# Kernel optimization log

Measured on AMD Instinct MI355X. Metric: run time of the kernel, lower is better.

The kernel has to match this reference:

```python
import jax, jax.numpy as jnp
import numpy as np

NUM_HEADS = 12

def _elu1(x):
    return jax.nn.elu(x) + 1.0

def setup_inputs() -> dict:
    key = jax.random.key(0)
    ks = jax.random.split(key, 7)
    B, Nq, Nk, D = 8, 4096, 1024, 768
    s = 0.02
    return {
        "x_query": jax.random.normal(ks[0], (B, Nq, D), dtype=jnp.float32),
        "x_key_value": jax.random.normal(ks[1], (B, Nk, D), dtype=jnp.float32),
        "Wq": jax.random.normal(ks[2], (D, D), dtype=jnp.float32) * s,
        "Wk": jax.random.normal(ks[3], (D, D), dtype=jnp.float32) * s,
        "Wv": jax.random.normal(ks[4], (D, D), dtype=jnp.float32) * s,
        "Wo": jax.random.normal(ks[5], (D, D), dtype=jnp.float32) * s,
        "bo": jax.random.normal(ks[6], (D,), dtype=jnp.float32) * s,
    }

def reference(x_query, x_key_value, Wq, Wk, Wv, Wo, bo):
    B, Nq, D = x_query.shape
    Nk = x_key_value.shape[1]
    H = NUM_HEADS
    hd = D // H
    # projections (torch Linear: x @ W.T), split heads -> [B, H, N, hd]
    q = (x_query @ Wq.T).reshape(B, Nq, H, hd).transpose(0, 2, 1, 3)
    k = (x_key_value @ Wk.T).reshape(B, Nk, H, hd).transpose(0, 2, 1, 3)
    v = (x_key_value @ Wv.T).reshape(B, Nk, H, hd).transpose(0, 2, 1, 3)
    q = _elu1(q)
    k = _elu1(k)
    # kv: [B,H,hd,hd]; k_sum: [B,H,hd]
    kv = jnp.einsum('bhnd,bhne->bhde', k, v)
    k_sum = k.sum(axis=2)
    z = 1.0 / (jnp.einsum('bhqd,bhd->bhq', q, k_sum) + 1e-6)  # [B,H,Nq]
    attn_out = jnp.einsum('bhqd,bhde->bhqe', q, kv) * z[..., None]
    attn_out = attn_out.transpose(0, 2, 1, 3).reshape(B, Nq, D)
    return attn_out @ Wo.T + bo
```

## Files before the change

### kernel.cpp

```cpp
#include <hip/hip_runtime.h>

typedef _Float16 half8_t __attribute__((ext_vector_type(8)));
typedef _Float16 half4_t __attribute__((ext_vector_type(4)));
typedef float    float4_t __attribute__((ext_vector_type(4)));

#define DIM 768

#define GLOAD16(g, l) __builtin_amdgcn_global_load_lds(                        \
    (const __attribute__((address_space(1))) void*)(g),                        \
    (__attribute__((address_space(3))) void*)(l), 16, 0, 0)

#define MFMA16(a, b, c) __builtin_amdgcn_mfma_f32_16x16x32_f16((a), (b), (c), 0, 0, 0)

__global__ __launch_bounds__(256) void cast_f32_f16(const float* __restrict__ s,
                                                    _Float16* __restrict__ d, int n8)
{
    int i = blockIdx.x * 256 + threadIdx.x;
    if (i < n8) {
        float4_t f0 = *(const float4_t*)&s[(size_t)i * 8];
        float4_t f1 = *(const float4_t*)&s[(size_t)i * 8 + 4];
        half8_t h;
        #pragma unroll
        for (int e = 0; e < 4; ++e) { h[e] = (_Float16)f0[e]; h[e + 4] = (_Float16)f1[e]; }
        *(half8_t*)&d[(size_t)i * 8] = h;
    }
}

__global__ __launch_bounds__(256) void cast4_f32_f16(
    const float* __restrict__ s0, const float* __restrict__ s1,
    const float* __restrict__ s2, const float* __restrict__ s3,
    _Float16* __restrict__ d0, _Float16* __restrict__ d1,
    _Float16* __restrict__ d2, _Float16* __restrict__ d3)
{
    const float* s; _Float16* d;
    switch (blockIdx.y) {
        case 0: s = s0; d = d0; break;
        case 1: s = s1; d = d1; break;
        case 2: s = s2; d = d2; break;
        default: s = s3; d = d3; break;
    }
    int i = blockIdx.x * 256 + threadIdx.x;
    float4_t f0 = *(const float4_t*)&s[(size_t)i * 8];
    float4_t f1 = *(const float4_t*)&s[(size_t)i * 8 + 4];
    half8_t h;
    #pragma unroll
    for (int e = 0; e < 4; ++e) { h[e] = (_Float16)f0[e]; h[e + 4] = (_Float16)f1[e]; }
    *(half8_t*)&d[(size_t)i * 8] = h;
}

__device__ __forceinline__ void gemm_core(const _Float16* __restrict__ A,
                                          const _Float16* __restrict__ W,
                                          int row0, int col0, _Float16* lds,
                                          float4_t acc[4][4])
{
    const int tid  = threadIdx.x;
    const int wid  = tid >> 6, lane = tid & 63;
    const int wr   = wid >> 1;
    const int wc   = wid & 1;

    const int srow  = lane & 15;
    const int skoct = lane >> 4;
    const _Float16* As0 = A + (size_t)(row0 + wid * 32 + srow)      * DIM + skoct * 8;
    const _Float16* As1 = A + (size_t)(row0 + wid * 32 + 16 + srow) * DIM + skoct * 8;
    const _Float16* Bs0 = W + (size_t)(col0 + wid * 16 + srow)      * DIM + skoct * 8;

#define STAGE(t, s) do {                                                      \
        GLOAD16(As0 + (t) * 32, &lds[(s) * 12288 + (2 * wid) * 512]);         \
        GLOAD16(As1 + (t) * 32, &lds[(s) * 12288 + (2 * wid + 1) * 512]);     \
        GLOAD16(Bs0 + (t) * 32, &lds[(s) * 12288 + 8192 + wid * 512]);        \
    } while (0)

    const int aoff = (wr * 4) * 512 + lane * 8;
    const int boff = 8192 + (wc * 4) * 512 + lane * 8;

    STAGE(0, 0);
    STAGE(1, 1);
    asm volatile("s_waitcnt vmcnt(3)" ::: "memory");
    __builtin_amdgcn_s_barrier();
    __builtin_amdgcn_sched_barrier(0);

    int s = 0, s2 = 2;
    for (int t = 0; t < 24; ++t) {
        const _Float16* sl = &lds[s * 12288];
        half8_t af[4], bf[4];
        #pragma unroll
        for (int mi = 0; mi < 4; ++mi)
            af[mi] = *(const half8_t*)&sl[aoff + mi * 512];
        #pragma unroll
        for (int ni = 0; ni < 4; ++ni)
            bf[ni] = *(const half8_t*)&sl[boff + ni * 512];
        if (t < 22) STAGE(t + 2, s2);

        __builtin_amdgcn_s_setprio(1);
        #pragma unroll
        for (int mi = 0; mi < 4; ++mi)
            #pragma unroll
            for (int ni = 0; ni < 4; ++ni)
                acc[mi][ni] = MFMA16(af[mi], bf[ni], acc[mi][ni]);
        __builtin_amdgcn_s_setprio(0);

        if (t < 23) {
            __builtin_amdgcn_sched_barrier(0);
            if (t < 22) asm volatile("s_waitcnt vmcnt(3)" ::: "memory");
            else        asm volatile("s_waitcnt vmcnt(0)" ::: "memory");
            __builtin_amdgcn_s_barrier();
            __builtin_amdgcn_sched_barrier(0);
        }
        s  = (s  == 2) ? 0 : s  + 1;
        s2 = (s2 == 2) ? 0 : s2 + 1;
    }
#undef STAGE
}

__global__ __launch_bounds__(512, 4) void proj_qkv(
    const _Float16* __restrict__ xq16, const _Float16* __restrict__ xkv16,
    const _Float16* __restrict__ Wq16, const _Float16* __restrict__ Wk16,
    const _Float16* __restrict__ Wv16,
    _Float16* __restrict__ q16, _Float16* __restrict__ k16,
    _Float16* __restrict__ v16)
{
    __shared__ __align__(16) _Float16 lds[3 * 12288];

    const int cpx = gridDim.x >> 3;
    int bid = (blockIdx.x & 7) * cpx + (blockIdx.x >> 3);

    const _Float16 *A, *W;
    _Float16 *O;
    bool elu;
    int brow, bcol;
    if (bid < 768) {
        A = xq16; W = Wq16; O = q16; elu = true;
        brow = bid / 6; bcol = bid - brow * 6;
    } else {
        int u = bid - 768;
        int mat = u / 192;  u -= mat * 192;
        A = xkv16; W = mat ? Wv16 : Wk16; O = mat ? v16 : k16; elu = !mat;
        brow = u / 6; bcol = u - brow * 6;
    }
    const int row0 = brow * 256, col0 = bcol * 128;

    float4_t acc[4][4] = {};
    gemm_core(A, W, row0, col0, lds, acc);

    const int wid = threadIdx.x >> 6, lane = threadIdx.x & 63;
    const int wr = wid >> 1, wc = wid & 1, lr = lane & 15, lkg = lane >> 4;
    #pragma unroll
    for (int mi = 0; mi < 4; ++mi) {
        #pragma unroll
        for (int ni = 0; ni < 4; ++ni) {
            #pragma unroll
            for (int e = 0; e < 4; ++e) {
                int r = row0 + wr * 64 + mi * 16 + lkg * 4 + e;
                int c = col0 + wc * 64 + ni * 16 + lr;
                float v = acc[mi][ni][e];
                if (elu) v = (v > 0.0f) ? (v + 1.0f) : __expf(v);
                O[(size_t)r * DIM + c] = (_Float16)v;
            }
        }
    }
}

__global__ __launch_bounds__(512, 4) void out_proj(
    const _Float16* __restrict__ a16, const _Float16* __restrict__ Wo16,
    const float* __restrict__ bo, float* __restrict__ out)
{
    __shared__ __align__(16) _Float16 lds[3 * 12288];

    const int cpx = gridDim.x >> 3;
    int bid = (blockIdx.x & 7) * cpx + (blockIdx.x >> 3);
    const int brow = bid / 6, bcol = bid - brow * 6;
    const int row0 = brow * 256, col0 = bcol * 128;

    float4_t acc[4][4] = {};
    gemm_core(a16, Wo16, row0, col0, lds, acc);

    const int wid = threadIdx.x >> 6, lane = threadIdx.x & 63;
    const int wr = wid >> 1, wc = wid & 1, lr = lane & 15, lkg = lane >> 4;
    #pragma unroll
    for (int mi = 0; mi < 4; ++mi) {
        #pragma unroll
        for (int ni = 0; ni < 4; ++ni) {
            #pragma unroll
            for (int e = 0; e < 4; ++e) {
                int r = row0 + wr * 64 + mi * 16 + lkg * 4 + e;
                int c = col0 + wc * 64 + ni * 16 + lr;
                out[(size_t)r * DIM + c] = acc[mi][ni][e] + bo[c];
            }
        }
    }
}

__global__ __launch_bounds__(256) void kv_reduce(const _Float16* __restrict__ k16,
                                                 const _Float16* __restrict__ v16,
                                                 float* __restrict__ kvh,
                                                 float* __restrict__ ksum)
{
    __shared__ __align__(16) _Float16 K[128][64];
    __shared__ __align__(16) _Float16 V[128][64];
    const int chunk = blockIdx.x;
    const int bh    = blockIdx.y;
    const int b = bh / 12, h = bh % 12;
    const int tid = threadIdx.x;

    const size_t base = ((size_t)b * 1024 + (size_t)chunk * 128) * DIM + h * 64;
    #pragma unroll
    for (int j = 0; j < 4; ++j) {
        int idx = j * 256 + tid;
        int r = idx >> 3, c = (idx & 7) * 8;
        *(half8_t*)&K[r][c] = *(const half8_t*)&k16[base + (size_t)r * DIM + c];
        *(half8_t*)&V[r][c] = *(const half8_t*)&v16[base + (size_t)r * DIM + c];
    }
    __syncthreads();

    const int d0 = (tid & 15) * 4;
    const int e0 = (tid >> 4) * 4;
    float acc[4][4] = {};
    #pragma unroll 4
    for (int n = 0; n < 128; ++n) {
        half4_t kd = *(const half4_t*)&K[n][d0];
        half4_t ve = *(const half4_t*)&V[n][e0];
        #pragma unroll
        for (int i = 0; i < 4; ++i)
            #pragma unroll
            for (int j = 0; j < 4; ++j)
                acc[i][j] += (float)ve[i] * (float)kd[j];
    }
    float* kvp = kvh + (size_t)bh * 64 * 64;
    #pragma unroll
    for (int i = 0; i < 4; ++i)
        #pragma unroll
        for (int j = 0; j < 4; ++j)
            atomicAdd(&kvp[(e0 + i) * 64 + d0 + j], acc[i][j]);

    if (tid < 64) {
        float s = 0.0f;
        for (int n = 0; n < 128; ++n) s += (float)K[n][tid];
        atomicAdd(&ksum[bh * 64 + tid], s);
    }
}

__global__ __launch_bounds__(256) void attn_kernel(_Float16* __restrict__ q16,
                                                   const float* __restrict__ kvh,
                                                   const float* __restrict__ ksum)
{
    __shared__ __align__(16) _Float16 Q[128][72];
    __shared__ __align__(16) _Float16 Bv[64][72];
    __shared__ float S[64];
    __shared__ float Z[128];

    const int h    = blockIdx.x;
    const int rb   = blockIdx.y;
    const int row0 = rb * 128;
    const int b    = row0 >> 12;
    const int bh   = b * 12 + h;
    const int tid  = threadIdx.x;

    #pragma unroll
    for (int j = 0; j < 4; ++j) {
        int idx = j * 256 + tid;
        int r = idx >> 3, c = (idx & 7) * 8;
        *(half8_t*)&Q[r][c] =
            *(const half8_t*)&q16[(size_t)(row0 + r) * DIM + h * 64 + c];
    }
    #pragma unroll
    for (int j = 0; j < 4; ++j) {
        int idx = j * 256 + tid;
        int r = idx >> 4, c = (idx & 15) * 4;
        float4_t f = *(const float4_t*)&kvh[((size_t)bh * 64 + r) * 64 + c];
        half4_t hh;
        #pragma unroll
        for (int e = 0; e < 4; ++e) hh[e] = (_Float16)f[e];
        *(half4_t*)&Bv[r][c] = hh;
    }
    if (tid < 64) S[tid] = ksum[bh * 64 + tid];
    __syncthreads();

    if (tid < 128) {
        float dot = 0.0f;
        #pragma unroll 8
        for (int d = 0; d < 64; ++d) dot += (float)Q[tid][d] * S[d];
        Z[tid] = 1.0f / (dot + 1e-6f);
    }
    __syncthreads();

    const int w = tid >> 6, lane = tid & 63;
    const int lr = lane & 15, lkg = lane >> 4;
    float4_t acc[2][4] = {};
    #pragma unroll
    for (int kc = 0; kc < 2; ++kc) {
        half8_t aF[2], bF[4];
        #pragma unroll
        for (int mi = 0; mi < 2; ++mi)
            aF[mi] = *(const half8_t*)&Q[w * 32 + mi * 16 + lr][kc * 32 + lkg * 8];
        #pragma unroll
        for (int ni = 0; ni < 4; ++ni)
            bF[ni] = *(const half8_t*)&Bv[ni * 16 + lr][kc * 32 + lkg * 8];
        #pragma unroll
        for (int mi = 0; mi < 2; ++mi)
            #pragma unroll
            for (int ni = 0; ni < 4; ++ni)
                acc[mi][ni] = MFMA16(aF[mi], bF[ni], acc[mi][ni]);
    }
    #pragma unroll
    for (int mi = 0; mi < 2; ++mi) {
        #pragma unroll
        for (int ni = 0; ni < 4; ++ni) {
            #pragma unroll
            for (int e = 0; e < 4; ++e) {
                int r = w * 32 + mi * 16 + lkg * 4 + e;
                float v = acc[mi][ni][e] * Z[r];
                q16[(size_t)(row0 + r) * DIM + h * 64 + ni * 16 + lr] = (_Float16)v;
            }
        }
    }
}

extern "C" void kernel_launch(void* const* d_in, const int* in_sizes, int n_in,
                              void* d_out, int out_size, void* d_ws, size_t ws_size,
                              hipStream_t stream)
{
    const float* xq  = (const float*)d_in[0];
    const float* xkv = (const float*)d_in[1];
    const float* Wq  = (const float*)d_in[2];
    const float* Wk  = (const float*)d_in[3];
    const float* Wv  = (const float*)d_in[4];
    const float* Wo  = (const float*)d_in[5];
    const float* bo  = (const float*)d_in[6];

    char* ws = (char*)d_ws;
    const size_t SZ_XKV16 = (size_t)8192 * 768 * 2;
    const size_t SZ_Q16   = (size_t)32768 * 768 * 2;
    const size_t SZ_W16   = (size_t)768 * 768 * 2;
    const size_t SZ_KVH   = (size_t)96 * 64 * 64 * 4;
    const size_t SZ_KSUM  = (size_t)96 * 64 * 4;

    _Float16* xkv16 = (_Float16*)(ws);
    _Float16* q16   = (_Float16*)(ws + SZ_XKV16);
    _Float16* Wq16  = (_Float16*)(ws + SZ_XKV16 + SZ_Q16);
    _Float16* Wk16  = (_Float16*)(ws + SZ_XKV16 + SZ_Q16 + SZ_W16);
    _Float16* Wv16  = (_Float16*)(ws + SZ_XKV16 + SZ_Q16 + 2 * SZ_W16);
    _Float16* Wo16  = (_Float16*)(ws + SZ_XKV16 + SZ_Q16 + 3 * SZ_W16);
    float*    kvh   = (float*)   (ws + SZ_XKV16 + SZ_Q16 + 4 * SZ_W16);
    float*    ksum  = (float*)   (ws + SZ_XKV16 + SZ_Q16 + 4 * SZ_W16 + SZ_KVH);

    char* ob = (char*)d_out;
    _Float16* xq16 = (_Float16*)(ob);
    _Float16* k16  = (_Float16*)(ob + 50331648);
    _Float16* v16  = (_Float16*)(ob + 50331648 + 12582912);
    float*    out  = (float*)d_out;

    cast_f32_f16<<<12288, 256, 0, stream>>>(xq,  xq16,  3145728);
    cast_f32_f16<<< 3072, 256, 0, stream>>>(xkv, xkv16,  786432);
    cast4_f32_f16<<<dim3(288, 4), 256, 0, stream>>>(Wq, Wk, Wv, Wo,
                                                    Wq16, Wk16, Wv16, Wo16);
    hipMemsetAsync(kvh, 0, SZ_KVH + SZ_KSUM, stream);

    proj_qkv<<<1152, 512, 0, stream>>>(xq16, xkv16, Wq16, Wk16, Wv16,
                                       q16, k16, v16);

    kv_reduce<<<dim3(8, 96), 256, 0, stream>>>(k16, v16, kvh, ksum);
    attn_kernel<<<dim3(12, 256), 256, 0, stream>>>(q16, kvh, ksum);

    out_proj<<<768, 512, 0, stream>>>(q16, Wo16, bo, out);
}
```

Measured before the change: 259.9 us.

## Fuse fp32-to-fp16 activation cast into projection GEMM and retile to 64-wide K steps

Drops the separate cast kernels for x_query and x_key_value. The QKV projection GEMM now loads fp32 activations straight into registers, converts them to fp16 and writes them to LDS itself, which removes a full round trip of the large activation tensors through global memory. The GEMM core is also restructured: K steps are 64 wide, warps are laid out 2x4 with 8x2 accumulators, double LDS buffers are larger, and the occupancy hint is removed. The cost is higher register and LDS pressure, extra barriers per tile, and manual conversion work sitting inside the main loop.

```diff
diff --git a/kernel.cpp b/kernel.cpp
--- a/kernel.cpp
+++ b/kernel.cpp
@@ -11,20 +11,6 @@
     (__attribute__((address_space(3))) void*)(l), 16, 0, 0)
 
 #define MFMA16(a, b, c) __builtin_amdgcn_mfma_f32_16x16x32_f16((a), (b), (c), 0, 0, 0)
-
-__global__ __launch_bounds__(256) void cast_f32_f16(const float* __restrict__ s,
-                                                    _Float16* __restrict__ d, int n8)
-{
-    int i = blockIdx.x * 256 + threadIdx.x;
-    if (i < n8) {
-        float4_t f0 = *(const float4_t*)&s[(size_t)i * 8];
-        float4_t f1 = *(const float4_t*)&s[(size_t)i * 8 + 4];
-        half8_t h;
-        #pragma unroll
-        for (int e = 0; e < 4; ++e) { h[e] = (_Float16)f0[e]; h[e + 4] = (_Float16)f1[e]; }
-        *(half8_t*)&d[(size_t)i * 8] = h;
-    }
-}
 
 __global__ __launch_bounds__(256) void cast4_f32_f16(
     const float* __restrict__ s0, const float* __restrict__ s1,
@@ -48,110 +34,253 @@
     *(half8_t*)&d[(size_t)i * 8] = h;
 }
 
-__device__ __forceinline__ void gemm_core(const _Float16* __restrict__ A,
+template<bool AF32>
+__device__ __forceinline__ void gemm_core(const void* __restrict__ Av,
                                           const _Float16* __restrict__ W,
-                                          int row0, int col0, _Float16* lds,
-                                          float4_t acc[4][4])
+                                          int row0, int col0,
+                                          _Float16* lds, float4_t acc[8][2])
 {
     const int tid  = threadIdx.x;
     const int wid  = tid >> 6, lane = tid & 63;
-    const int wr   = wid >> 1;
-    const int wc   = wid & 1;
-
-    const int srow  = lane & 15;
-    const int skoct = lane >> 4;
-    const _Float16* As0 = A + (size_t)(row0 + wid * 32 + srow)      * DIM + skoct * 8;
-    const _Float16* As1 = A + (size_t)(row0 + wid * 32 + 16 + srow) * DIM + skoct * 8;
-    const _Float16* Bs0 = W + (size_t)(col0 + wid * 16 + srow)      * DIM + skoct * 8;
-
-#define STAGE(t, s) do {                                                      \
-        GLOAD16(As0 + (t) * 32, &lds[(s) * 12288 + (2 * wid) * 512]);         \
-        GLOAD16(As1 + (t) * 32, &lds[(s) * 12288 + (2 * wid + 1) * 512]);     \
-        GLOAD16(Bs0 + (t) * 32, &lds[(s) * 12288 + 8192 + wid * 512]);        \
-    } while (0)
-
-    const int aoff = (wr * 4) * 512 + lane * 8;
-    const int boff = 8192 + (wc * 4) * 512 + lane * 8;
-
-    STAGE(0, 0);
-    STAGE(1, 1);
-    asm volatile("s_waitcnt vmcnt(3)" ::: "memory");
-    __builtin_amdgcn_s_barrier();
-    __builtin_amdgcn_sched_barrier(0);
-
-    int s = 0, s2 = 2;
-    for (int t = 0; t < 24; ++t) {
-        const _Float16* sl = &lds[s * 12288];
-        half8_t af[4], bf[4];
-        #pragma unroll
-        for (int mi = 0; mi < 4; ++mi)
-            af[mi] = *(const half8_t*)&sl[aoff + mi * 512];
-        #pragma unroll
-        for (int ni = 0; ni < 4; ++ni)
-            bf[ni] = *(const half8_t*)&sl[boff + ni * 512];
-        if (t < 22) STAGE(t + 2, s2);
-
-        __builtin_amdgcn_s_setprio(1);
-        #pragma unroll
-        for (int mi = 0; mi < 4; ++mi)
-            #pragma unroll
-            for (int ni = 0; ni < 4; ++ni)
-                acc[mi][ni] = MFMA16(af[mi], bf[ni], acc[mi][ni]);
-        __builtin_amdgcn_s_setprio(0);
-
-        if (t < 23) {
+    const int wr   = wid >> 2, wc = wid & 3;
+
+    const _Float16* Bst = W + (size_t)(col0 + wid * 16 + (lane & 15)) * DIM
+                            + (lane >> 4) * 8;
+
+    const int aoffs = (wr * 8) * 1024 + lane * 8;
+    const int boffs = 16384 + (wc * 2) * 1024 + lane * 8;
+
+    const _Float16* Ah = nullptr;
+    const float*    Af = nullptr;
+    int awr = 0;
+    if constexpr (AF32) {
+        const int rg = 2 * wid + (lane >> 5);
+        const int j  = lane & 31;
+        const int row = j & 15, q = j >> 4;
+        Af  = (const float*)Av + (size_t)(row0 + rg * 16 + row) * DIM + q * 32;
+        awr = (rg * 2 + q) * 512 + row * 8;
+    } else {
+        Ah = (const _Float16*)Av + (size_t)(row0 + 2 * wid * 16 + (lane & 15)) * DIM
+                                 + (lane >> 4) * 8;
+    }
+
+#define B_STAGE(t, s) do {                                                     \
+        GLOAD16(Bst + (t) * 64,      &lds[(s) * 24576 + 16384 + (2*wid  ) * 512]); \
+        GLOAD16(Bst + (t) * 64 + 32, &lds[(s) * 24576 + 16384 + (2*wid+1) * 512]); \
+    } while (0)
+
+#define AH_STAGE(t, s) do {                                                    \
+        GLOAD16(Ah + (t)*64,              &lds[(s)*24576 + (4*wid  )*512]);    \
+        GLOAD16(Ah + (t)*64 + 32,         &lds[(s)*24576 + (4*wid+1)*512]);    \
+        GLOAD16(Ah + (t)*64 + 16*DIM,     &lds[(s)*24576 + (4*wid+2)*512]);    \
+        GLOAD16(Ah + (t)*64 + 16*DIM+32,  &lds[(s)*24576 + (4*wid+3)*512]);    \
+    } while (0)
+
+#define AF_ISSUE(t, R) do { _Pragma("unroll")                                  \
+        for (int i = 0; i < 8; ++i)                                            \
+            R[i] = *(const float4_t*)(Af + (t) * 64 + i * 4);                  \
+    } while (0)
+
+#define AF_WRITE(s1w, R) do {                                                  \
+        _Float16* dst = &lds[(s1w) * 24576 + awr];                             \
+        _Pragma("unroll") for (int p = 0; p < 4; ++p) {                        \
+            half8_t h;                                                         \
+            _Pragma("unroll") for (int e = 0; e < 4; ++e) {                    \
+                h[e] = (_Float16)R[2*p][e]; h[4+e] = (_Float16)R[2*p+1][e]; }  \
+            *(half8_t*)&dst[p * 128] = h; }                                    \
+    } while (0)
+
+#define READ_BF(s) do {                                                        \
+        bf[0][0] = *(const half8_t*)&lds[(s)*24576 + boffs];                   \
+        bf[0][1] = *(const half8_t*)&lds[(s)*24576 + boffs + 512];             \
+        bf[1][0] = *(const half8_t*)&lds[(s)*24576 + boffs + 1024];            \
+        bf[1][1] = *(const half8_t*)&lds[(s)*24576 + boffs + 1536];            \
+    } while (0)
+
+#define READ_AFR(af, s, mb) do { _Pragma("unroll")                             \
+        for (int i = 0; i < 4; ++i) {                                          \
+            af[i][0] = *(const half8_t*)&lds[(s)*24576 + aoffs + ((mb)+i)*1024];       \
+            af[i][1] = *(const half8_t*)&lds[(s)*24576 + aoffs + ((mb)+i)*1024 + 512]; \
+        } } while (0)
+
+#define MMA4(base, af) do {                                                    \
+        asm volatile("s_waitcnt lgkmcnt(0)" ::: "memory");                     \
+        __builtin_amdgcn_sched_barrier(0);                                     \
+        __builtin_amdgcn_s_setprio(1);                                         \
+        _Pragma("unroll") for (int i = 0; i < 4; ++i)                          \
+            _Pragma("unroll") for (int n2 = 0; n2 < 2; ++n2) {                 \
+                acc[(base)+i][n2] = MFMA16(af[i][0], bf[n2][0], acc[(base)+i][n2]); \
+                acc[(base)+i][n2] = MFMA16(af[i][1], bf[n2][1], acc[(base)+i][n2]); \
+            }                                                                  \
+        __builtin_amdgcn_s_setprio(0);                                         \
+        __builtin_amdgcn_sched_barrier(0);                                     \
+    } while (0)
+
+    if constexpr (AF32) {
+        float4_t Ra[8], Rb[8];
+        AF_ISSUE(0, Ra); B_STAGE(0, 0);
+        __builtin_amdgcn_sched_barrier(0);
+        AF_ISSUE(1, Rb); B_STAGE(1, 1);
+        __builtin_amdgcn_sched_barrier(0);
+        asm volatile("s_waitcnt vmcnt(10)" ::: "memory");
+        AF_WRITE(0, Ra);
+        asm volatile("s_waitcnt lgkmcnt(0)" ::: "memory");
+        __builtin_amdgcn_sched_barrier(0);
+        __builtin_amdgcn_s_barrier();
+
+#define TILE_F32(t, Ri, Rw) do {                                               \
+        const int s = (t) % 3, s1 = ((t)+1) % 3, s2 = ((t)+2) % 3;             \
+        __builtin_amdgcn_sched_barrier(0);                                     \
+        half8_t bf[2][2];                                                      \
+        READ_BF(s);                                                            \
+        { half8_t af[4][2]; READ_AFR(af, s, 0);                                \
+          AF_ISSUE((t)+2, Ri); B_STAGE((t)+2, s2);                             \
+          __builtin_amdgcn_s_barrier();                                        \
+          MMA4(0, af);                                                         \
+          __builtin_amdgcn_s_barrier(); }                                      \
+        { half8_t af[4][2]; READ_AFR(af, s, 4);                                \
+          asm volatile("s_waitcnt vmcnt(10)" ::: "memory");                    \
+          AF_WRITE(s1, Rw);                                                    \
+          __builtin_amdgcn_s_barrier();                                        \
+          MMA4(4, af);                                                         \
+          __builtin_amdgcn_s_barrier(); }                                      \
+    } while (0)
+
+        #pragma unroll
+        for (int t = 0; t < 10; t += 2) {
+            TILE_F32(t,     Ra, Rb);
+            TILE_F32(t + 1, Rb, Ra);
+        }
+        {
             __builtin_amdgcn_sched_barrier(0);
-            if (t < 22) asm volatile("s_waitcnt vmcnt(3)" ::: "memory");
-            else        asm volatile("s_waitcnt vmcnt(0)" ::: "memory");
-            __builtin_amdgcn_s_barrier();
+            half8_t bf[2][2];
+            READ_BF(1);
+            { half8_t af[4][2]; READ_AFR(af, 1, 0);
+              __builtin_amdgcn_s_barrier();
+              MMA4(0, af);
+              __builtin_amdgcn_s_barrier(); }
+            { half8_t af[4][2]; READ_AFR(af, 1, 4);
+              asm volatile("s_waitcnt vmcnt(0)" ::: "memory");
+              AF_WRITE(2, Rb);
+              __builtin_amdgcn_s_barrier();
+              MMA4(4, af);
+              __builtin_amdgcn_s_barrier(); }
+        }
+        {
             __builtin_amdgcn_sched_barrier(0);
-        }
-        s  = (s  == 2) ? 0 : s  + 1;
-        s2 = (s2 == 2) ? 0 : s2 + 1;
-    }
-#undef STAGE
-}
-
-__global__ __launch_bounds__(512, 4) void proj_qkv(
-    const _Float16* __restrict__ xq16, const _Float16* __restrict__ xkv16,
+            half8_t bf[2][2];
+            READ_BF(2);
+            { half8_t af[4][2]; READ_AFR(af, 2, 0);
+              __builtin_amdgcn_s_barrier();
+              MMA4(0, af);
+              __builtin_amdgcn_s_barrier(); }
+            { half8_t af[4][2]; READ_AFR(af, 2, 4);
+              __builtin_amdgcn_s_barrier();
+              MMA4(4, af); }
+        }
+#undef TILE_F32
+    } else {
+        AH_STAGE(0, 0); B_STAGE(0, 0);
+        __builtin_amdgcn_sched_barrier(0);
+        AH_STAGE(1, 1); B_STAGE(1, 1);
+        __builtin_amdgcn_sched_barrier(0);
+        asm volatile("s_waitcnt vmcnt(6)" ::: "memory");
+        __builtin_amdgcn_s_barrier();
+
+#define TILE_H16(t) do {                                                       \
+        const int s = (t) % 3, s2 = ((t)+2) % 3;                               \
+        __builtin_amdgcn_sched_barrier(0);                                     \
+        half8_t bf[2][2];                                                      \
+        READ_BF(s);                                                            \
+        { half8_t af[4][2]; READ_AFR(af, s, 0);                                \
+          AH_STAGE((t)+2, s2); B_STAGE((t)+2, s2);                             \
+          __builtin_amdgcn_s_barrier();                                        \
+          MMA4(0, af);                                                         \
+          __builtin_amdgcn_s_barrier(); }                                      \
+        { half8_t af[4][2]; READ_AFR(af, s, 4);                                \
+          __builtin_amdgcn_s_barrier();                                        \
+          MMA4(4, af);                                                         \
+          asm volatile("s_waitcnt vmcnt(6)" ::: "memory");                     \
+          __builtin_amdgcn_s_barrier(); }                                      \
+    } while (0)
+
+        #pragma unroll
+        for (int t = 0; t < 10; ++t) TILE_H16(t);
+        {
+            __builtin_amdgcn_sched_barrier(0);
+            half8_t bf[2][2];
+            READ_BF(1);
+            { half8_t af[4][2]; READ_AFR(af, 1, 0);
+              __builtin_amdgcn_s_barrier();
+              MMA4(0, af);
+              __builtin_amdgcn_s_barrier(); }
+            { half8_t af[4][2]; READ_AFR(af, 1, 4);
+              __builtin_amdgcn_s_barrier();
+              MMA4(4, af);
+              asm volatile("s_waitcnt vmcnt(0)" ::: "memory");
+              __builtin_amdgcn_s_barrier(); }
+        }
+        {
+            __builtin_amdgcn_sched_barrier(0);
+            half8_t bf[2][2];
+            READ_BF(2);
+            { half8_t af[4][2]; READ_AFR(af, 2, 0);
+              __builtin_amdgcn_s_barrier();
+              MMA4(0, af);
+              __builtin_amdgcn_s_barrier(); }
+            { half8_t af[4][2]; READ_AFR(af, 2, 4);
+              __builtin_amdgcn_s_barrier();
+              MMA4(4, af); }
+        }
+#undef TILE_H16
+    }
+#undef B_STAGE
+#undef AH_STAGE
+#undef AF_ISSUE
+#undef AF_WRITE
+#undef READ_BF
+#undef READ_AFR
+#undef MMA4
+}
+
+__global__ __launch_bounds__(512) void proj_qkv(
+    const float* __restrict__ xq, const float* __restrict__ xkv,
     const _Float16* __restrict__ Wq16, const _Float16* __restrict__ Wk16,
     const _Float16* __restrict__ Wv16,
     _Float16* __restrict__ q16, _Float16* __restrict__ k16,
     _Float16* __restrict__ v16)
 {
-    __shared__ __align__(16) _Float16 lds[3 * 12288];
+    __shared__ __align__(16) _Float16 lds[3 * 24576];
 
     const int cpx = gridDim.x >> 3;
     int bid = (blockIdx.x & 7) * cpx + (blockIdx.x >> 3);
 
-    const _Float16 *A, *W;
-    _Float16 *O;
-    bool elu;
+    const float* A; const _Float16* W; _Float16* O; bool elu;
     int brow, bcol;
     if (bid < 768) {
-        A = xq16; W = Wq16; O = q16; elu = true;
+        A = xq; W = Wq16; O = q16; elu = true;
         brow = bid / 6; bcol = bid - brow * 6;
     } else {
         int u = bid - 768;
         int mat = u / 192;  u -= mat * 192;
-        A = xkv16; W = mat ? Wv16 : Wk16; O = mat ? v16 : k16; elu = !mat;
+        A = xkv; W = mat ? Wv16 : Wk16; O = mat ? v16 : k16; elu = !mat;
         brow = u / 6; bcol = u - brow * 6;
     }
     const int row0 = brow * 256, col0 = bcol * 128;
 
-    float4_t acc[4][4] = {};
-    gemm_core(A, W, row0, col0, lds, acc);
+    float4_t acc[8][2] = {};
+    gemm_core<true>(A, W, row0, col0, lds, acc);
 
     const int wid = threadIdx.x >> 6, lane = threadIdx.x & 63;
-    const int wr = wid >> 1, wc = wid & 1, lr = lane & 15, lkg = lane >> 4;
-    #pragma unroll
-    for (int mi = 0; mi < 4; ++mi) {
-        #pragma unroll
-        for (int ni = 0; ni < 4; ++ni) {
+    const int wr = wid >> 2, wc = wid & 3, lr = lane & 15, lkg = lane >> 4;
+    #pragma unroll
+    for (int mi = 0; mi < 8; ++mi) {
+        #pragma unroll
+        for (int ni = 0; ni < 2; ++ni) {
             #pragma unroll
             for (int e = 0; e < 4; ++e) {
-                int r = row0 + wr * 64 + mi * 16 + lkg * 4 + e;
-                int c = col0 + wc * 64 + ni * 16 + lr;
+                int r = row0 + wr * 128 + mi * 16 + lkg * 4 + e;
+                int c = col0 + wc * 32 + ni * 16 + lr;
                 float v = acc[mi][ni][e];
                 if (elu) v = (v > 0.0f) ? (v + 1.0f) : __expf(v);
                 O[(size_t)r * DIM + c] = (_Float16)v;
@@ -160,30 +289,30 @@
     }
 }
 
-__global__ __launch_bounds__(512, 4) void out_proj(
+__global__ __launch_bounds__(512) void out_proj(
     const _Float16* __restrict__ a16, const _Float16* __restrict__ Wo16,
     const float* __restrict__ bo, float* __restrict__ out)
 {
-    __shared__ __align__(16) _Float16 lds[3 * 12288];
+    __shared__ __align__(16) _Float16 lds[3 * 24576];
 
     const int cpx = gridDim.x >> 3;
     int bid = (blockIdx.x & 7) * cpx + (blockIdx.x >> 3);
     const int brow = bid / 6, bcol = bid - brow * 6;
     const int row0 = brow * 256, col0 = bcol * 128;
 
-    float4_t acc[4][4] = {};
-    gemm_core(a16, Wo16, row0, col0, lds, acc);
+    float4_t acc[8][2] = {};
+    gemm_core<false>(a16, Wo16, row0, col0, lds, acc);
 
     const int wid = threadIdx.x >> 6, lane = threadIdx.x & 63;
-    const int wr = wid >> 1, wc = wid & 1, lr = lane & 15, lkg = lane >> 4;
-    #pragma unroll
-    for (int mi = 0; mi < 4; ++mi) {
-        #pragma unroll
-        for (int ni = 0; ni < 4; ++ni) {
+    const int wr = wid >> 2, wc = wid & 3, lr = lane & 15, lkg = lane >> 4;
+    #pragma unroll
+    for (int mi = 0; mi < 8; ++mi) {
+        #pragma unroll
+        for (int ni = 0; ni < 2; ++ni) {
             #pragma unroll
             for (int e = 0; e < 4; ++e) {
-                int r = row0 + wr * 64 + mi * 16 + lkg * 4 + e;
-                int c = col0 + wc * 64 + ni * 16 + lr;
+                int r = row0 + wr * 128 + mi * 16 + lkg * 4 + e;
+                int c = col0 + wc * 32 + ni * 16 + lr;
                 out[(size_t)r * DIM + c] = acc[mi][ni][e] + bo[c];
             }
         }
@@ -328,34 +457,29 @@
     const float* bo  = (const float*)d_in[6];
 
     char* ws = (char*)d_ws;
-    const size_t SZ_XKV16 = (size_t)8192 * 768 * 2;
-    const size_t SZ_Q16   = (size_t)32768 * 768 * 2;
-    const size_t SZ_W16   = (size_t)768 * 768 * 2;
-    const size_t SZ_KVH   = (size_t)96 * 64 * 64 * 4;
-    const size_t SZ_KSUM  = (size_t)96 * 64 * 4;
-
-    _Float16* xkv16 = (_Float16*)(ws);
-    _Float16* q16   = (_Float16*)(ws + SZ_XKV16);
-    _Float16* Wq16  = (_Float16*)(ws + SZ_XKV16 + SZ_Q16);
-    _Float16* Wk16  = (_Float16*)(ws + SZ_XKV16 + SZ_Q16 + SZ_W16);
-    _Float16* Wv16  = (_Float16*)(ws + SZ_XKV16 + SZ_Q16 + 2 * SZ_W16);
-    _Float16* Wo16  = (_Float16*)(ws + SZ_XKV16 + SZ_Q16 + 3 * SZ_W16);
-    float*    kvh   = (float*)   (ws + SZ_XKV16 + SZ_Q16 + 4 * SZ_W16);
-    float*    ksum  = (float*)   (ws + SZ_XKV16 + SZ_Q16 + 4 * SZ_W16 + SZ_KVH);
+    const size_t SZ_Q16  = (size_t)32768 * 768 * 2;
+    const size_t SZ_W16  = (size_t)768 * 768 * 2;
+    const size_t SZ_KVH  = (size_t)96 * 64 * 64 * 4;
+    const size_t SZ_KSUM = (size_t)96 * 64 * 4;
+
+    _Float16* q16  = (_Float16*)(ws);
+    _Float16* Wq16 = (_Float16*)(ws + SZ_Q16);
+    _Float16* Wk16 = (_Float16*)(ws + SZ_Q16 + SZ_W16);
+    _Float16* Wv16 = (_Float16*)(ws + SZ_Q16 + 2 * SZ_W16);
+    _Float16* Wo16 = (_Float16*)(ws + SZ_Q16 + 3 * SZ_W16);
+    float*    kvh  = (float*)   (ws + SZ_Q16 + 4 * SZ_W16);
+    float*    ksum = (float*)   (ws + SZ_Q16 + 4 * SZ_W16 + SZ_KVH);
 
     char* ob = (char*)d_out;
-    _Float16* xq16 = (_Float16*)(ob);
-    _Float16* k16  = (_Float16*)(ob + 50331648);
-    _Float16* v16  = (_Float16*)(ob + 50331648 + 12582912);
-    float*    out  = (float*)d_out;
-
-    cast_f32_f16<<<12288, 256, 0, stream>>>(xq,  xq16,  3145728);
-    cast_f32_f16<<< 3072, 256, 0, stream>>>(xkv, xkv16,  786432);
+    _Float16* k16 = (_Float16*)(ob + 50331648);
+    _Float16* v16 = (_Float16*)(ob + 50331648 + 12582912);
+    float*    out = (float*)d_out;
+
     cast4_f32_f16<<<dim3(288, 4), 256, 0, stream>>>(Wq, Wk, Wv, Wo,
                                                     Wq16, Wk16, Wv16, Wo16);
     hipMemsetAsync(kvh, 0, SZ_KVH + SZ_KSUM, stream);
 
-    proj_qkv<<<1152, 512, 0, stream>>>(xq16, xkv16, Wq16, Wk16, Wv16,
+    proj_qkv<<<1152, 512, 0, stream>>>(xq, xkv, Wq16, Wk16, Wv16,
                                        q16, k16, v16);
 
     kv_reduce<<<dim3(8, 96), 256, 0, stream>>>(k16, v16, kvh, ksum);
```

New measurement: 338.5 us. +30.2%, slower.

## Restructure GEMM core to 128x128 tiles, BK=64 double buffering, 256 threads

Applied to the files above, without the earlier changes.

Reworks the shared GEMM core from 256x128 tiles with 512 threads, BK=32 and triple buffering to 128x128 tiles with 256 threads, BK=64 and a double-buffered LDS pipeline. Each wave now issues eight MFMAs per fragment pair per K step, and there are half as many barriers. Grid sizes for the projection and output GEMMs double to match. The two activation cast kernels are also merged into one launch. The risks are lower data reuse per block, a full vmcnt(0) wait before each barrier that reduces load/compute overlap, and different occupancy behaviour.

```diff
diff --git a/kernel.cpp b/kernel.cpp
--- a/kernel.cpp
+++ b/kernel.cpp
@@ -12,18 +12,21 @@
 
 #define MFMA16(a, b, c) __builtin_amdgcn_mfma_f32_16x16x32_f16((a), (b), (c), 0, 0, 0)
 
-__global__ __launch_bounds__(256) void cast_f32_f16(const float* __restrict__ s,
-                                                    _Float16* __restrict__ d, int n8)
+__global__ __launch_bounds__(256) void cast_acts(const float* __restrict__ xq,
+                                                 const float* __restrict__ xkv,
+                                                 _Float16* __restrict__ dq,
+                                                 _Float16* __restrict__ dkv)
 {
     int i = blockIdx.x * 256 + threadIdx.x;
-    if (i < n8) {
-        float4_t f0 = *(const float4_t*)&s[(size_t)i * 8];
-        float4_t f1 = *(const float4_t*)&s[(size_t)i * 8 + 4];
-        half8_t h;
-        #pragma unroll
-        for (int e = 0; e < 4; ++e) { h[e] = (_Float16)f0[e]; h[e + 4] = (_Float16)f1[e]; }
-        *(half8_t*)&d[(size_t)i * 8] = h;
-    }
+    const float* s; _Float16* d; int off;
+    if (i < 3145728) { s = xq;  d = dq;  off = i; }
+    else             { s = xkv; d = dkv; off = i - 3145728; }
+    float4_t f0 = *(const float4_t*)&s[(size_t)off * 8];
+    float4_t f1 = *(const float4_t*)&s[(size_t)off * 8 + 4];
+    half8_t h;
+    #pragma unroll
+    for (int e = 0; e < 4; ++e) { h[e] = (_Float16)f0[e]; h[e + 4] = (_Float16)f1[e]; }
+    *(half8_t*)&d[(size_t)off * 8] = h;
 }
 
 __global__ __launch_bounds__(256) void cast4_f32_f16(
@@ -50,94 +53,97 @@
 
 __device__ __forceinline__ void gemm_core(const _Float16* __restrict__ A,
                                           const _Float16* __restrict__ W,
-                                          int row0, int col0, _Float16* lds,
-                                          float4_t acc[4][4])
+                                          int row0, int col0,
+                                          _Float16* lds, float4_t acc[4][4])
 {
     const int tid  = threadIdx.x;
     const int wid  = tid >> 6, lane = tid & 63;
-    const int wr   = wid >> 1;
-    const int wc   = wid & 1;
-
-    const int srow  = lane & 15;
-    const int skoct = lane >> 4;
-    const _Float16* As0 = A + (size_t)(row0 + wid * 32 + srow)      * DIM + skoct * 8;
-    const _Float16* As1 = A + (size_t)(row0 + wid * 32 + 16 + srow) * DIM + skoct * 8;
-    const _Float16* Bs0 = W + (size_t)(col0 + wid * 16 + srow)      * DIM + skoct * 8;
-
-#define STAGE(t, s) do {                                                      \
-        GLOAD16(As0 + (t) * 32, &lds[(s) * 12288 + (2 * wid) * 512]);         \
-        GLOAD16(As1 + (t) * 32, &lds[(s) * 12288 + (2 * wid + 1) * 512]);     \
-        GLOAD16(Bs0 + (t) * 32, &lds[(s) * 12288 + 8192 + wid * 512]);        \
+    const int wr   = wid >> 1, wc = wid & 1;
+
+    const _Float16* Ast[4];
+    const _Float16* Bst[4];
+    #pragma unroll
+    for (int j = 0; j < 4; ++j) {
+        const int rr = (2 * wid + (j >> 1)) * 16 + (lane & 15);
+        const int k0 = (j & 1) * 32 + (lane >> 4) * 8;
+        Ast[j] = A + (size_t)(row0 + rr) * DIM + k0;
+        Bst[j] = W + (size_t)(col0 + rr) * DIM + k0;
+    }
+
+#define STAGE(t, s) do { _Pragma("unroll")                                     \
+        for (int j = 0; j < 4; ++j)                                            \
+            GLOAD16(Ast[j] + (t) * 64, &lds[(s) * 16384 + (4*wid + j) * 512]); \
+        _Pragma("unroll")                                                      \
+        for (int j = 0; j < 4; ++j)                                            \
+            GLOAD16(Bst[j] + (t) * 64,                                         \
+                    &lds[(s) * 16384 + 8192 + (4*wid + j) * 512]);             \
     } while (0)
 
-    const int aoff = (wr * 4) * 512 + lane * 8;
-    const int boff = 8192 + (wc * 4) * 512 + lane * 8;
-
     STAGE(0, 0);
+    __builtin_amdgcn_sched_barrier(0);
     STAGE(1, 1);
-    asm volatile("s_waitcnt vmcnt(3)" ::: "memory");
+    asm volatile("s_waitcnt vmcnt(8)" ::: "memory");
     __builtin_amdgcn_s_barrier();
     __builtin_amdgcn_sched_barrier(0);
 
-    int s = 0, s2 = 2;
-    for (int t = 0; t < 24; ++t) {
-        const _Float16* sl = &lds[s * 12288];
-        half8_t af[4], bf[4];
+    #pragma unroll
+    for (int t = 0; t < 12; ++t) {
+        const int sb = (t & 1) * 16384;
+        half8_t af[4][2], bf[4][2];
+        #pragma unroll
+        for (int mi = 0; mi < 4; ++mi) {
+            af[mi][0] = *(const half8_t*)&lds[sb + ((wr*4 + mi)*2    )*512 + lane*8];
+            af[mi][1] = *(const half8_t*)&lds[sb + ((wr*4 + mi)*2 + 1)*512 + lane*8];
+        }
+        #pragma unroll
+        for (int ni = 0; ni < 4; ++ni) {
+            bf[ni][0] = *(const half8_t*)&lds[sb + 8192 + ((wc*4 + ni)*2    )*512 + lane*8];
+            bf[ni][1] = *(const half8_t*)&lds[sb + 8192 + ((wc*4 + ni)*2 + 1)*512 + lane*8];
+        }
+        __builtin_amdgcn_s_setprio(1);
         #pragma unroll
         for (int mi = 0; mi < 4; ++mi)
-            af[mi] = *(const half8_t*)&sl[aoff + mi * 512];
-        #pragma unroll
-        for (int ni = 0; ni < 4; ++ni)
-            bf[ni] = *(const half8_t*)&sl[boff + ni * 512];
-        if (t < 22) STAGE(t + 2, s2);
-
-        __builtin_amdgcn_s_setprio(1);
-        #pragma unroll
-        for (int mi = 0; mi < 4; ++mi)
-            #pragma unroll
-            for (int ni = 0; ni < 4; ++ni)
-                acc[mi][ni] = MFMA16(af[mi], bf[ni], acc[mi][ni]);
+            #pragma unroll
+            for (int ni = 0; ni < 4; ++ni) {
+                acc[mi][ni] = MFMA16(af[mi][0], bf[ni][0], acc[mi][ni]);
+                acc[mi][ni] = MFMA16(af[mi][1], bf[ni][1], acc[mi][ni]);
+            }
         __builtin_amdgcn_s_setprio(0);
 
-        if (t < 23) {
-            __builtin_amdgcn_sched_barrier(0);
-            if (t < 22) asm volatile("s_waitcnt vmcnt(3)" ::: "memory");
-            else        asm volatile("s_waitcnt vmcnt(0)" ::: "memory");
+        if (t < 11) {
+            asm volatile("s_waitcnt vmcnt(0)" ::: "memory");
             __builtin_amdgcn_s_barrier();
             __builtin_amdgcn_sched_barrier(0);
-        }
-        s  = (s  == 2) ? 0 : s  + 1;
-        s2 = (s2 == 2) ? 0 : s2 + 1;
+            if (t < 10) STAGE(t + 2, t & 1);
+        }
     }
 #undef STAGE
 }
 
-__global__ __launch_bounds__(512, 4) void proj_qkv(
+__global__ __launch_bounds__(256, 2) void proj_qkv(
     const _Float16* __restrict__ xq16, const _Float16* __restrict__ xkv16,
     const _Float16* __restrict__ Wq16, const _Float16* __restrict__ Wk16,
     const _Float16* __restrict__ Wv16,
     _Float16* __restrict__ q16, _Float16* __restrict__ k16,
     _Float16* __restrict__ v16)
 {
-    __shared__ __align__(16) _Float16 lds[3 * 12288];
+    __shared__ __align__(16) _Float16 lds[2 * 16384];
 
     const int cpx = gridDim.x >> 3;
     int bid = (blockIdx.x & 7) * cpx + (blockIdx.x >> 3);
 
-    const _Float16 *A, *W;
-    _Float16 *O;
-    bool elu;
+    const _Float16 *A, *W; _Float16* O; bool elu;
     int brow, bcol;
-    if (bid < 768) {
+    if (bid < 1536) {
         A = xq16; W = Wq16; O = q16; elu = true;
         brow = bid / 6; bcol = bid - brow * 6;
     } else {
-        int u = bid - 768;
-        int mat = u / 192;  u -= mat * 192;
+        int u = bid - 1536;
+        int mat = u / 384;  u -= mat * 384;
         A = xkv16; W = mat ? Wv16 : Wk16; O = mat ? v16 : k16; elu = !mat;
         brow = u / 6; bcol = u - brow * 6;
     }
-    const int row0 = brow * 256, col0 = bcol * 128;
+    const int row0 = brow * 128, col0 = bcol * 128;
 
     float4_t acc[4][4] = {};
     gemm_core(A, W, row0, col0, lds, acc);
@@ -160,16 +166,16 @@
     }
 }
 
-__global__ __launch_bounds__(512, 4) void out_proj(
+__global__ __launch_bounds__(256, 2) void out_proj(
     const _Float16* __restrict__ a16, const _Float16* __restrict__ Wo16,
     const float* __restrict__ bo, float* __restrict__ out)
 {
-    __shared__ __align__(16) _Float16 lds[3 * 12288];
+    __shared__ __align__(16) _Float16 lds[2 * 16384];
 
     const int cpx = gridDim.x >> 3;
     int bid = (blockIdx.x & 7) * cpx + (blockIdx.x >> 3);
     const int brow = bid / 6, bcol = bid - brow * 6;
-    const int row0 = brow * 256, col0 = bcol * 128;
+    const int row0 = brow * 128, col0 = bcol * 128;
 
     float4_t acc[4][4] = {};
     gemm_core(a16, Wo16, row0, col0, lds, acc);
@@ -328,20 +334,20 @@
     const float* bo  = (const float*)d_in[6];
 
     char* ws = (char*)d_ws;
+    const size_t SZ_Q16   = (size_t)32768 * 768 * 2;
     const size_t SZ_XKV16 = (size_t)8192 * 768 * 2;
-    const size_t SZ_Q16   = (size_t)32768 * 768 * 2;
     const size_t SZ_W16   = (size_t)768 * 768 * 2;
     const size_t SZ_KVH   = (size_t)96 * 64 * 64 * 4;
     const size_t SZ_KSUM  = (size_t)96 * 64 * 4;
 
-    _Float16* xkv16 = (_Float16*)(ws);
-    _Float16* q16   = (_Float16*)(ws + SZ_XKV16);
-    _Float16* Wq16  = (_Float16*)(ws + SZ_XKV16 + SZ_Q16);
-    _Float16* Wk16  = (_Float16*)(ws + SZ_XKV16 + SZ_Q16 + SZ_W16);
-    _Float16* Wv16  = (_Float16*)(ws + SZ_XKV16 + SZ_Q16 + 2 * SZ_W16);
-    _Float16* Wo16  = (_Float16*)(ws + SZ_XKV16 + SZ_Q16 + 3 * SZ_W16);
-    float*    kvh   = (float*)   (ws + SZ_XKV16 + SZ_Q16 + 4 * SZ_W16);
-    float*    ksum  = (float*)   (ws + SZ_XKV16 + SZ_Q16 + 4 * SZ_W16 + SZ_KVH);
+    _Float16* q16   = (_Float16*)(ws);
+    _Float16* xkv16 = (_Float16*)(ws + SZ_Q16);
+    _Float16* Wq16  = (_Float16*)(ws + SZ_Q16 + SZ_XKV16);
+    _Float16* Wk16  = (_Float16*)(ws + SZ_Q16 + SZ_XKV16 + SZ_W16);
+    _Float16* Wv16  = (_Float16*)(ws + SZ_Q16 + SZ_XKV16 + 2 * SZ_W16);
+    _Float16* Wo16  = (_Float16*)(ws + SZ_Q16 + SZ_XKV16 + 3 * SZ_W16);
+    float*    kvh   = (float*)   (ws + SZ_Q16 + SZ_XKV16 + 4 * SZ_W16);
+    float*    ksum  = (float*)   (ws + SZ_Q16 + SZ_XKV16 + 4 * SZ_W16 + SZ_KVH);
 
     char* ob = (char*)d_out;
     _Float16* xq16 = (_Float16*)(ob);
@@ -349,17 +355,16 @@
     _Float16* v16  = (_Float16*)(ob + 50331648 + 12582912);
     float*    out  = (float*)d_out;
 
-    cast_f32_f16<<<12288, 256, 0, stream>>>(xq,  xq16,  3145728);
-    cast_f32_f16<<< 3072, 256, 0, stream>>>(xkv, xkv16,  786432);
+    cast_acts<<<15360, 256, 0, stream>>>(xq, xkv, xq16, xkv16);
     cast4_f32_f16<<<dim3(288, 4), 256, 0, stream>>>(Wq, Wk, Wv, Wo,
                                                     Wq16, Wk16, Wv16, Wo16);
     hipMemsetAsync(kvh, 0, SZ_KVH + SZ_KSUM, stream);
 
-    proj_qkv<<<1152, 512, 0, stream>>>(xq16, xkv16, Wq16, Wk16, Wv16,
+    proj_qkv<<<2304, 256, 0, stream>>>(xq16, xkv16, Wq16, Wk16, Wv16,
                                        q16, k16, v16);
 
     kv_reduce<<<dim3(8, 96), 256, 0, stream>>>(k16, v16, kvh, ksum);
     attn_kernel<<<dim3(12, 256), 256, 0, stream>>>(q16, kvh, ksum);
 
-    out_proj<<<768, 512, 0, stream>>>(q16, Wo16, bo, out);
-}
+    out_proj<<<1536, 256, 0, stream>>>(q16, Wo16, bo, out);
+}
```

After: 292.6 us. 12.6% more time.
